# Performance work log

Hardware: AMD Instinct MI355X
Metric: run time of the kernel (lower is better)

## Reference

```python
import jax, jax.numpy as jnp
import numpy as np

B, C, F, H = 512, 80, 768, 256
EPS = 1e-5
THR = 0.5
SCALE = 1.0 / np.sqrt(H)


def _ln(z, g, b):
    m = jnp.mean(z, axis=-1, keepdims=True)
    v = jnp.mean((z - m) ** 2, axis=-1, keepdims=True)
    return (z - m) * jax.lax.rsqrt(v + EPS) * g + b


def setup_inputs() -> dict:
    key = jax.random.key(0)
    ks = jax.random.split(key, 12)
    w = 0.05  # weight scale for numerical sanity
    return {
        "x": jax.random.normal(ks[0], (B, C, H), jnp.float32),
        "visual_features": jax.random.normal(ks[1], (B, F), jnp.float32),
        "labels": jax.random.randint(ks[2], (B, C), 0, 2, jnp.int32),
        # visual_proj: Linear(F,H) + LayerNorm(H)
        "Wp": jax.random.normal(ks[3], (F, H), jnp.float32) * w,
        "bp": jnp.zeros((H,), jnp.float32),
        "gp": jnp.ones((H,), jnp.float32),
        "bep": jnp.zeros((H,), jnp.float32),
        # per-class extractors: stacked Linear(H,H) + LayerNorm(H)
        "Wc": jax.random.normal(ks[4], (C, H, H), jnp.float32) * w,
        "bc": jnp.zeros((C, H), jnp.float32),
        "gc": jnp.ones((C, H), jnp.float32),
        "bec": jnp.zeros((C, H), jnp.float32),
        # attention projections
        "Wq": jax.random.normal(ks[5], (H, H), jnp.float32) * w,
        "bq": jnp.zeros((H,), jnp.float32),
        "Wk": jax.random.normal(ks[6], (H, H), jnp.float32) * w,
        "bk": jnp.zeros((H,), jnp.float32),
        "Wv": jax.random.normal(ks[7], (H, H), jnp.float32) * w,
        "bv": jnp.zeros((H,), jnp.float32),
        "Wo": jax.random.normal(ks[8], (H, H), jnp.float32) * w,
        "bo": jnp.zeros((H,), jnp.float32),
    }


def reference(x, visual_features, labels, Wp, bp, gp, bep, Wc, bc, gc, bec,
              Wq, bq, Wk, bk, Wv, bv, Wo, bo):
    # visual_proj: Linear + LN + ReLU  -> (B,H)
    vis = jax.nn.relu(_ln(visual_features @ Wp + bp, gp, bep))
    # per-class extractor ensemble fused into one batched GEMM -> (B,C,H)
    z = jnp.einsum('bh,chk->bck', vis, Wc) + bc
    class_feats = jax.nn.relu(_ln(z, gc, bec))
    x = x + class_feats
    q = x @ Wq + bq
    k = x @ Wk + bk
    v = x @ Wv + bv
    scores = jnp.einsum('bch,bdh->bcd', q, k) * SCALE  # (B,C,C)
    scores = scores * (scores > THR).astype(scores.dtype)  # hard similarity mask
    label_mask = labels.astype(scores.dtype)[:, None, :] * 0.8 + 0.2
    scores = scores * label_mask
    attn = jax.nn.softmax(scores, axis=-1)
    out = jnp.einsum('bcd,bdh->bch', attn, v)
    return out @ Wo + bo
```

## Files before the change

### kernel.cpp

```cpp
#include <hip/hip_runtime.h>
#include <hip/hip_bf16.h>
#include <math.h>

#define Bq 512
#define Cq 80
#define Fq 768
#define Hq 256

constexpr float EPS   = 1e-5f;
constexpr float THR   = 0.5f;
constexpr float SCALE = 0.0625f;

using f32x4 = __attribute__((ext_vector_type(4))) float;
using s16x8 = __attribute__((ext_vector_type(8))) short;
using s16x4 = __attribute__((ext_vector_type(4))) short;

#define MFMA16 __builtin_amdgcn_mfma_f32_16x16x32_bf16


__device__ __forceinline__ float waveReduceSum(float v) {
#pragma unroll
  for (int m = 32; m >= 1; m >>= 1) v += __shfl_xor(v, m);
  return v;
}

__device__ __forceinline__ float bfu(unsigned short v) {
  return __uint_as_float(((unsigned)v) << 16);
}

__device__ __forceinline__ unsigned short f2bf(float f) {
  __hip_bfloat16 h = __float2bfloat16(f);
  return *reinterpret_cast<unsigned short*>(&h);
}

__device__ __forceinline__ int packOff(int tile, int kk8, int g, int l15, int e) {
  return ((tile * 8 + kk8) * 4 + g) * 128 + l15 * 8 + e;
}

__global__ __launch_bounds__(256) void k_setup(
    const float* __restrict__ vf, const float* __restrict__ Wp,
    const float* __restrict__ bp, const float* __restrict__ gp,
    const float* __restrict__ bep,
    unsigned short* __restrict__ visPh, unsigned short* __restrict__ visPl,
    const float* __restrict__ Wq, const float* __restrict__ Wk,
    const float* __restrict__ bq, const float* __restrict__ bk,
    unsigned short* __restrict__ MTph, unsigned short* __restrict__ MTpl,
    float* __restrict__ w1, float* __restrict__ w2, float* __restrict__ cqk,
    const float* __restrict__ Wc, const float* __restrict__ Wv,
    const float* __restrict__ Wo,
    unsigned short* __restrict__ WcTph, unsigned short* __restrict__ WcTpl,
    unsigned short* __restrict__ WvTp, unsigned short* __restrict__ WoTp) {
  __shared__ float smA[Fq];
  __shared__ float red[4], redB[4], redC[4];
  const int blk = blockIdx.x;

  if (blk < 512) {
    const int b = blk, h = threadIdx.x;
    for (int i = h; i < Fq; i += 256) smA[i] = vf[b * Fq + i];
    __syncthreads();
    float acc = bp[h];
    for (int f = 0; f < Fq; f++) acc = fmaf(smA[f], Wp[f * Hq + h], acc);
    const int w = h >> 6, lane = h & 63;
    float s = waveReduceSum(acc);
    if (lane == 0) red[w] = s;
    __syncthreads();
    const float mean = (red[0] + red[1] + red[2] + red[3]) * (1.0f / Hq);
    __syncthreads();
    const float d = acc - mean;
    s = waveReduceSum(d * d);
    if (lane == 0) red[w] = s;
    __syncthreads();
    const float var = (red[0] + red[1] + red[2] + red[3]) * (1.0f / Hq);
    float y = d * rsqrtf(var + EPS) * gp[h] + bep[h];
    y = fmaxf(y, 0.0f);
    const unsigned short hb = f2bf(y);
    const int off = packOff(b >> 4, h >> 5, (h & 31) >> 3, b & 15, h & 7);
    visPh[off] = hb;
    visPl[off] = f2bf(y - bfu(hb));
  } else if (blk < 768) {
    const int i = blk - 512, j = threadIdx.x;
    const int wv = j >> 6, lane = j & 63;
    smA[j] = Wq[i * Hq + j];
    __syncthreads();
    float acc = 0.f;
    const float* wkr = Wk + (size_t)j * Hq;
    for (int h = 0; h < Hq; h += 4) {
      const float4 a = *reinterpret_cast<const float4*>(&smA[h]);
      const float4 bb = *reinterpret_cast<const float4*>(&wkr[h]);
      acc = fmaf(a.x, bb.x, fmaf(a.y, bb.y, fmaf(a.z, bb.z, fmaf(a.w, bb.w, acc))));
    }
    const unsigned short hb = f2bf(acc);
    const int off = packOff(j >> 4, i >> 5, (i & 31) >> 3, j & 15, i & 7);
    MTph[off] = hb;
    MTpl[off] = f2bf(acc - bfu(hb));
    float p1 = smA[j] * bk[j];
    float p2 = Wk[(size_t)i * Hq + j] * bq[j];
    float p3 = bq[j] * bk[j];
    p1 = waveReduceSum(p1);
    p2 = waveReduceSum(p2);
    p3 = waveReduceSum(p3);
    if (lane == 0) { red[wv] = p1; redB[wv] = p2; redC[wv] = p3; }
    __syncthreads();
    if (j == 0) {
      w1[i] = red[0] + red[1] + red[2] + red[3];
      w2[i] = redB[0] + redB[1] + redB[2] + redB[3];
      if (i == 0) *cqk = redC[0] + redC[1] + redC[2] + redC[3];
    }
  } else {
    const int NWc = Cq * 32 * 256;
    const int NTOT = NWc + 2 * 32 * 256;
    for (int idx = (blk - 768) * 256 + threadIdx.x; idx < NTOT; idx += 1024 * 256) {
      if (idx < NWc) {
        const int c = idx >> 13, k8 = (idx >> 8) & 31, n = idx & 255;
        const float* src = Wc + (size_t)c * 65536 + (size_t)k8 * 8 * 256 + n;
        s16x8 hh, ll;
#pragma unroll
        for (int e = 0; e < 8; e++) {
          const float v = src[e * 256];
          const unsigned short hb = f2bf(v);
          hh[e] = (short)hb;
          ll[e] = (short)f2bf(v - bfu(hb));
        }
        const int off = c * 65536 + packOff(n >> 4, k8 >> 2, k8 & 3, n & 15, 0);
        *reinterpret_cast<s16x8*>(WcTph + off) = hh;
        *reinterpret_cast<s16x8*>(WcTpl + off) = ll;
      } else {
        const int r = idx - NWc;
        const int which = r >> 13;
        const int r2 = r & 8191;
        const int k8 = r2 >> 8, n = r2 & 255;
        const float* src = (which == 0 ? Wv : Wo) + (size_t)k8 * 8 * 256 + n;
        s16x8 hh;
#pragma unroll
        for (int e = 0; e < 8; e++) hh[e] = (short)f2bf(src[e * 256]);
        const int off = packOff(n >> 4, k8 >> 2, k8 & 3, n & 15, 0);
        *reinterpret_cast<s16x8*>((which == 0 ? WvTp : WoTp) + off) = hh;
      }
    }
  }
}

__global__ __launch_bounds__(256) void k_gemm1f(
    const unsigned short* __restrict__ visPh, const unsigned short* __restrict__ visPl,
    const unsigned short* __restrict__ WcTph, const unsigned short* __restrict__ WcTpl,
    const float* __restrict__ x, const float* __restrict__ bc,
    const float* __restrict__ gc, const float* __restrict__ bec,
    const float* __restrict__ w1, const float* __restrict__ w2,
    unsigned short* __restrict__ Xgh, unsigned short* __restrict__ Xgl,
    float* __restrict__ u, float* __restrict__ vv) {
  const int blk = blockIdx.x;
  const int mapped = (blk & 7) * 160 + (blk >> 3);
  const int c = mapped >> 4;
  const int bx = mapped & 15;
  const int b0 = bx * 32;
  const int tid = threadIdx.x;
  const int wvi = tid >> 6, lane = tid & 63;
  const int l15 = lane & 15, l4 = lane >> 4;

  __shared__ float Zs[32][268];

  f32x4 acc[2][4];
#pragma unroll
  for (int m = 0; m < 2; m++)
#pragma unroll
    for (int n = 0; n < 4; n++) acc[m][n] = (f32x4){0.f, 0.f, 0.f, 0.f};

  const unsigned short* Bh = WcTph + (size_t)c * 65536;
  const unsigned short* Bl = WcTpl + (size_t)c * 65536;

  for (int kk8 = 0; kk8 < 8; kk8++) {
    s16x8 ah[2], al[2], bh[4], bl[4];
#pragma unroll
    for (int m = 0; m < 2; m++) {
      const int off = packOff(bx * 2 + m, kk8, l4, l15, 0);
      ah[m] = *reinterpret_cast<const s16x8*>(visPh + off);
      al[m] = *reinterpret_cast<const s16x8*>(visPl + off);
    }
#pragma unroll
    for (int n = 0; n < 4; n++) {
      const int off = packOff(wvi * 4 + n, kk8, l4, l15, 0);
      bh[n] = *reinterpret_cast<const s16x8*>(Bh + off);
      bl[n] = *reinterpret_cast<const s16x8*>(Bl + off);
    }
#pragma unroll
    for (int m = 0; m < 2; m++)
#pragma unroll
      for (int n = 0; n < 4; n++) {
        acc[m][n] = MFMA16(ah[m], bh[n], acc[m][n], 0, 0, 0);
        acc[m][n] = MFMA16(ah[m], bl[n], acc[m][n], 0, 0, 0);
        acc[m][n] = MFMA16(al[m], bh[n], acc[m][n], 0, 0, 0);
      }
  }

#pragma unroll
  for (int m = 0; m < 2; m++)
#pragma unroll
    for (int n = 0; n < 4; n++) {
      const int col = wvi * 64 + n * 16 + l15;
      const float bcv = bc[c * Hq + col];
#pragma unroll
      for (int r = 0; r < 4; r++)
        Zs[m * 16 + l4 * 4 + r][col] = acc[m][n][r] + bcv;
    }
  __syncthreads();

  const int row = tid >> 3, sub = tid & 7;
  const int grow = b0 + row;
  const size_t xrow = ((size_t)grow * Cq + c) * Hq;
  float zz[32];
  float sum = 0.f, sumsq = 0.f;
#pragma unroll
  for (int kq = 0; kq < 8; kq++) {
    const float4 z = *reinterpret_cast<const float4*>(&Zs[row][sub * 4 + kq * 32]);
    zz[4 * kq + 0] = z.x; zz[4 * kq + 1] = z.y;
    zz[4 * kq + 2] = z.z; zz[4 * kq + 3] = z.w;
    sum += z.x + z.y + z.z + z.w;
    sumsq += z.x * z.x + z.y * z.y + z.z * z.z + z.w * z.w;
  }
#pragma unroll
  for (int msk = 4; msk >= 1; msk >>= 1) {
    sum += __shfl_xor(sum, msk);
    sumsq += __shfl_xor(sumsq, msk);
  }
  const float mean = sum * (1.0f / Hq);
  const float var = sumsq * (1.0f / Hq) - mean * mean;
  const float inv = rsqrtf(var + EPS);

  float pu = 0.f, pv = 0.f;
#pragma unroll
  for (int kq = 0; kq < 8; kq++) {
    const int col = sub * 4 + kq * 32;
    const float4 xv = *reinterpret_cast<const float4*>(&x[xrow + col]);
    const float xr[4] = {xv.x, xv.y, xv.z, xv.w};
    s16x4 hh, ll;
#pragma unroll
    for (int e = 0; e < 4; e++) {
      float tt = (zz[4 * kq + e] - mean) * inv * gc[c * Hq + col + e] + bec[c * Hq + col + e];
      tt = fmaxf(tt, 0.f);
      const float xp = xr[e] + tt;
      const unsigned short hb2 = f2bf(xp);
      hh[e] = (short)hb2;
      ll[e] = (short)f2bf(xp - bfu(hb2));
      pu = fmaf(xp, w1[col + e], pu);
      pv = fmaf(xp, w2[col + e], pv);
    }
    *reinterpret_cast<s16x4*>(Xgh + xrow + col) = hh;
    *reinterpret_cast<s16x4*>(Xgl + xrow + col) = ll;
  }
#pragma unroll
  for (int msk = 4; msk >= 1; msk >>= 1) {
    pu += __shfl_xor(pu, msk);
    pv += __shfl_xor(pv, msk);
  }
  if (sub == 0) {
    u[(size_t)grow * Cq + c] = pu;
    vv[(size_t)grow * Cq + c] = pv;
  }
}

__global__ __launch_bounds__(256) void k_gemm2p(
    unsigned short* Xh, unsigned short* Xl,
    const unsigned short* __restrict__ MTph, const unsigned short* __restrict__ MTpl,
    const unsigned short* __restrict__ WvTp, const float* __restrict__ bv,
    unsigned short* __restrict__ XMh, unsigned short* __restrict__ XMl,
    unsigned short* __restrict__ Vt) {
  __shared__ __attribute__((aligned(16))) unsigned short Xsh[32 * 264];
  __shared__ __attribute__((aligned(16))) unsigned short Xsl[32 * 264];
  __shared__ __attribute__((aligned(16))) unsigned short XMsh[8192];
  __shared__ __attribute__((aligned(16))) unsigned short XMsl[8192];
  __shared__ __attribute__((aligned(16))) unsigned short Vst[256 * 24];

  const int blk = blockIdx.x;
  const int r0 = blk * 32;
  const int tid = threadIdx.x;
  const int wvi = tid >> 6, lane = tid & 63;
  const int l15 = lane & 15, l4 = lane >> 4;

#pragma unroll
  for (int it = 0; it < 4; it++) {
    const int ch = it * 256 + tid;
    const int rr = ch >> 5, cc = ch & 31;
    const size_t gsrc = (size_t)(r0 + rr) * Hq + cc * 8;
    *reinterpret_cast<s16x8*>(&Xsh[rr * 264 + cc * 8]) =
        *reinterpret_cast<const s16x8*>(Xh + gsrc);
    *reinterpret_cast<s16x8*>(&Xsl[rr * 264 + cc * 8]) =
        *reinterpret_cast<const s16x8*>(Xl + gsrc);
  }
  __syncthreads();

  f32x4 acc[2][4];
#pragma unroll
  for (int m = 0; m < 2; m++)
#pragma unroll
    for (int n = 0; n < 4; n++) acc[m][n] = (f32x4){0.f, 0.f, 0.f, 0.f};

  for (int kk8 = 0; kk8 < 8; kk8++) {
    s16x8 ah[2], al[2], bh[4], bl[4];
#pragma unroll
    for (int m = 0; m < 2; m++) {
      const int lo = (m * 16 + l15) * 264 + kk8 * 32 + l4 * 8;
      ah[m] = *reinterpret_cast<const s16x8*>(&Xsh[lo]);
      al[m] = *reinterpret_cast<const s16x8*>(&Xsl[lo]);
    }
#pragma unroll
    for (int n = 0; n < 4; n++) {
      const int off = packOff(wvi * 4 + n, kk8, l4, l15, 0);
      bh[n] = *reinterpret_cast<const s16x8*>(MTph + off);
      bl[n] = *reinterpret_cast<const s16x8*>(MTpl + off);
    }
#pragma unroll
    for (int m = 0; m < 2; m++)
#pragma unroll
      for (int n = 0; n < 4; n++) {
        acc[m][n] = MFMA16(ah[m], bh[n], acc[m][n], 0, 0, 0);
        acc[m][n] = MFMA16(ah[m], bl[n], acc[m][n], 0, 0, 0);
        acc[m][n] = MFMA16(al[m], bh[n], acc[m][n], 0, 0, 0);
      }
  }

#pragma unroll
  for (int m = 0; m < 2; m++)
#pragma unroll
    for (int n = 0; n < 4; n++) {
      const int col = wvi * 64 + n * 16 + l15;
      const int kk8c = col >> 5, gc = (col & 31) >> 3, ec = col & 7;
#pragma unroll
      for (int r = 0; r < 4; r++) {
        const int off = ((m * 8 + kk8c) * 4 + gc) * 128 + (l4 * 4 + r) * 8 + ec;
        const float v = acc[m][n][r];
        const unsigned short hb = f2bf(v);
        XMsh[off] = hb;
        XMsl[off] = f2bf(v - bfu(hb));
      }
    }
  __syncthreads();

#pragma unroll
  for (int it = 0; it < 4; it++) {
    const int ch = it * 256 + tid;
    const size_t gdst = (size_t)blk * 8192 + ch * 8;
    *reinterpret_cast<s16x8*>(XMh + gdst) = *reinterpret_cast<const s16x8*>(&XMsh[ch * 8]);
    *reinterpret_cast<s16x8*>(XMl + gdst) = *reinterpret_cast<const s16x8*>(&XMsl[ch * 8]);
    const int l15c = ch & 15, g3 = (ch >> 4) & 3, kk = (ch >> 6) & 7, mm = ch >> 9;
    const int lsrc = (mm * 16 + l15c) * 264 + kk * 32 + g3 * 8;
    *reinterpret_cast<s16x8*>(Xh + gdst) = *reinterpret_cast<const s16x8*>(&Xsh[lsrc]);
    *reinterpret_cast<s16x8*>(Xl + gdst) = *reinterpret_cast<const s16x8*>(&Xsl[lsrc]);
  }

  for (int m = 0; m < 2; m++) {
    f32x4 vac[4];
#pragma unroll
    for (int n = 0; n < 4; n++) vac[n] = (f32x4){0.f, 0.f, 0.f, 0.f};
    for (int kk8 = 0; kk8 < 8; kk8++) {
      const int lo = (m * 16 + l15) * 264 + kk8 * 32 + l4 * 8;
      const s16x8 ah = *reinterpret_cast<const s16x8*>(&Xsh[lo]);
      const s16x8 al = *reinterpret_cast<const s16x8*>(&Xsl[lo]);
#pragma unroll
      for (int n = 0; n < 4; n++) {
        const s16x8 bh = *reinterpret_cast<const s16x8*>(
            WvTp + packOff(wvi * 4 + n, kk8, l4, l15, 0));
        vac[n] = MFMA16(ah, bh, vac[n], 0, 0, 0);
        vac[n] = MFMA16(al, bh, vac[n], 0, 0, 0);
      }
    }
#pragma unroll
    for (int n = 0; n < 4; n++) {
      const int col = (wvi * 4 + n) * 16 + l15;
      const float bvv = bv[col];
#pragma unroll
      for (int r = 0; r < 4; r++)
        Vst[col * 24 + l4 * 4 + r] = f2bf(vac[n][r] + bvv);
    }
    __syncthreads();
    {
      const int gt = blk * 2 + m;
      const int bb = gt / 5, ct = gt - bb * 5;
      const unsigned short* src = &Vst[tid * 24];
      const s16x8 va = *reinterpret_cast<const s16x8*>(src);
      const s16x8 vb2 = *reinterpret_cast<const s16x8*>(src + 8);
      const size_t ga = ((size_t)bb * Hq + tid) * Cq + ct * 16;
      *reinterpret_cast<s16x8*>(Vt + ga) = va;
      *reinterpret_cast<s16x8*>(Vt + ga + 8) = vb2;
    }
    __syncthreads();
  }
}

__global__ __launch_bounds__(320) void k_attn5(
    const unsigned short* __restrict__ XPh, const unsigned short* __restrict__ XPl,
    const unsigned short* __restrict__ XMh, const unsigned short* __restrict__ XMl,
    const unsigned short* __restrict__ Vt, const int* __restrict__ labels,
    const float* __restrict__ u, const float* __restrict__ vv,
    const float* __restrict__ cqk, const unsigned short* __restrict__ WoTp,
    const float* __restrict__ bo, float* __restrict__ out) {
  __shared__ unsigned short Pl_[80][104];
  __shared__ unsigned short Olds[80][264];
  __shared__ float us[80], vvs[80], lms[80];

  const int b = blockIdx.x, t = threadIdx.x;
  const int w = t >> 6, lane = t & 63;
  const int l15 = lane & 15, g = lane >> 4;

  if (t < 80) {
    us[t] = u[b * Cq + t];
    vvs[t] = vv[b * Cq + t];
    lms[t] = (float)labels[b * Cq + t] * 0.8f + 0.2f;
  }

  f32x4 sacc[5];
#pragma unroll
  for (int mt = 0; mt < 5; mt++) sacc[mt] = (f32x4){0.f, 0.f, 0.f, 0.f};

  for (int kk8 = 0; kk8 < 8; kk8++) {
    const int offB = packOff(b * 5 + w, kk8, g, l15, 0);
    const s16x8 bh = *reinterpret_cast<const s16x8*>(XMh + offB);
    const s16x8 bl = *reinterpret_cast<const s16x8*>(XMl + offB);
#pragma unroll
    for (int mt = 0; mt < 5; mt++) {
      const int offA = packOff(b * 5 + mt, kk8, g, l15, 0);
      const s16x8 ah = *reinterpret_cast<const s16x8*>(XPh + offA);
      const s16x8 al = *reinterpret_cast<const s16x8*>(XPl + offA);
      sacc[mt] = MFMA16(ah, bh, sacc[mt], 0, 0, 0);
      sacc[mt] = MFMA16(ah, bl, sacc[mt], 0, 0, 0);
      sacc[mt] = MFMA16(al, bh, sacc[mt], 0, 0, 0);
    }
  }
  __syncthreads();

  const int i = 16 * w + l15;
  const float ui = us[i];
  const float cq = *cqk;
  float p[5][4];
  float mx = -1e30f;
#pragma unroll
  for (int mt = 0; mt < 5; mt++)
#pragma unroll
    for (int r = 0; r < 4; r++) {
      const int j = 16 * mt + 4 * g + r;
      float sc = (sacc[mt][r] + ui + vvs[j] + cq) * SCALE;
      sc = (sc > THR) ? sc : 0.0f;
      sc *= lms[j];
      p[mt][r] = sc;
      mx = fmaxf(mx, sc);
    }
  mx = fmaxf(mx, __shfl_xor(mx, 16));
  mx = fmaxf(mx, __shfl_xor(mx, 32));
  float sum = 0.f;
#pragma unroll
  for (int mt = 0; mt < 5; mt++)
#pragma unroll
    for (int r = 0; r < 4; r++) {
      const float e = __expf(p[mt][r] - mx);
      p[mt][r] = e;
      sum += e;
    }
  sum += __shfl_xor(sum, 16);
  sum += __shfl_xor(sum, 32);
  const float inv = 1.0f / sum;

#pragma unroll
  for (int mt = 0; mt < 5; mt++) {
    uint2 pk;
    pk.x = (unsigned)f2bf(p[mt][0] * inv) | ((unsigned)f2bf(p[mt][1] * inv) << 16);
    pk.y = (unsigned)f2bf(p[mt][2] * inv) | ((unsigned)f2bf(p[mt][3] * inv) << 16);
    *reinterpret_cast<uint2*>(reinterpret_cast<char*>(&Pl_[i][0]) + 32 * mt + 8 * g) = pk;
  }
  if (t < 160) {
    const uint4 z = {0u, 0u, 0u, 0u};
    *reinterpret_cast<uint4*>(reinterpret_cast<char*>(&Pl_[t >> 1][0]) + 160 + 16 * (t & 1)) = z;
  }
  __syncthreads();

  s16x8 pa[3];
#pragma unroll
  for (int ks = 0; ks < 3; ks++)
    pa[ks] = *reinterpret_cast<const s16x8*>(
        reinterpret_cast<const char*>(&Pl_[i][0]) + 64 * ks + 16 * g);

  f32x4 oacc[16];
#pragma unroll
  for (int n = 0; n < 16; n++) oacc[n] = (f32x4){0.f, 0.f, 0.f, 0.f};

  const size_t vbase = (size_t)b * Hq * Cq;
#pragma unroll 4
  for (int n = 0; n < 16; n++) {
    const size_t hrow = vbase + (size_t)(16 * n + l15) * Cq + 8 * g;
#pragma unroll
    for (int ks = 0; ks < 3; ks++) {
      const s16x8 vb = *reinterpret_cast<const s16x8*>(Vt + hrow + 32 * ks);
      oacc[n] = MFMA16(pa[ks], vb, oacc[n], 0, 0, 0);
    }
  }

#pragma unroll
  for (int n = 0; n < 16; n++)
#pragma unroll
    for (int r = 0; r < 4; r++)
      Olds[16 * w + 4 * g + r][16 * n + l15] = f2bf(oacc[n][r]);

  f32x4 acc2[16];
#pragma unroll
  for (int n = 0; n < 16; n++) acc2[n] = (f32x4){0.f, 0.f, 0.f, 0.f};

  for (int ks = 0; ks < 8; ks++) {
    const s16x8 af = *reinterpret_cast<const s16x8*>(
        reinterpret_cast<const char*>(&Olds[16 * w + l15][0]) + 64 * ks + 16 * g);
#pragma unroll
    for (int n = 0; n < 16; n++) {
      const s16x8 bf = *reinterpret_cast<const s16x8*>(WoTp + packOff(n, ks, g, l15, 0));
      acc2[n] = MFMA16(af, bf, acc2[n], 0, 0, 0);
    }
  }

#pragma unroll
  for (int n = 0; n < 16; n++) {
    const float bov = bo[16 * n + l15];
#pragma unroll
    for (int r = 0; r < 4; r++)
      out[((size_t)b * Cq + 16 * w + 4 * g + r) * Hq + 16 * n + l15] =
          acc2[n][r] + bov;
  }
}

extern "C" void kernel_launch(void* const* d_in, const int* in_sizes, int n_in,
                              void* d_out, int out_size, void* d_ws, size_t ws_size,
                              hipStream_t stream) {
  const float* x   = (const float*)d_in[0];
  const float* vf  = (const float*)d_in[1];
  const int*   lab = (const int*)d_in[2];
  const float* Wp  = (const float*)d_in[3];
  const float* bp  = (const float*)d_in[4];
  const float* gp  = (const float*)d_in[5];
  const float* bep = (const float*)d_in[6];
  const float* Wc  = (const float*)d_in[7];
  const float* bc  = (const float*)d_in[8];
  const float* gc  = (const float*)d_in[9];
  const float* bec = (const float*)d_in[10];
  const float* Wq  = (const float*)d_in[11];
  const float* bq_ = (const float*)d_in[12];
  const float* Wk  = (const float*)d_in[13];
  const float* bk_ = (const float*)d_in[14];
  const float* Wv  = (const float*)d_in[15];
  const float* bv_ = (const float*)d_in[16];
  const float* Wo  = (const float*)d_in[17];
  const float* bo_ = (const float*)d_in[18];
  float* out = (float*)d_out;
  (void)ws_size; (void)in_sizes; (void)n_in; (void)out_size;

  char* W = (char*)d_ws;
  unsigned short* Xh    = (unsigned short*)(W + 0);
  unsigned short* Xl    = (unsigned short*)(W + 20971520);
  unsigned short* WcTph = (unsigned short*)(W + 41943040);
  unsigned short* WcTpl = (unsigned short*)(W + 52428800);
  unsigned short* XMh   = (unsigned short*)(W + 41943040);
  unsigned short* XMl   = (unsigned short*)(W + 62914560);
  unsigned short* Vt    = (unsigned short*)(W + 83886080);
  unsigned short* visPh = (unsigned short*)(W + 104857600);
  unsigned short* visPl = (unsigned short*)(W + 105119744);
  unsigned short* MTph  = (unsigned short*)(W + 105381888);
  unsigned short* MTpl  = (unsigned short*)(W + 105512960);
  unsigned short* WvTp  = (unsigned short*)(W + 105644032);
  unsigned short* WoTp  = (unsigned short*)(W + 105775104);
  float* w1  = (float*)(W + 105906176);
  float* w2  = (float*)(W + 105907200);
  float* cqk = (float*)(W + 105908224);
  float* u   = (float*)(W + 105908480);
  float* vvv = (float*)(W + 106072320);

  k_setup<<<1792, 256, 0, stream>>>(vf, Wp, bp, gp, bep, visPh, visPl,
                                    Wq, Wk, bq_, bk_, MTph, MTpl, w1, w2, cqk,
                                    Wc, Wv, Wo, WcTph, WcTpl, WvTp, WoTp);
  k_gemm1f<<<1280, 256, 0, stream>>>(visPh, visPl, WcTph, WcTpl, x, bc, gc, bec,
                                     w1, w2, Xh, Xl, u, vvv);
  k_gemm2p<<<1280, 256, 0, stream>>>(Xh, Xl, MTph, MTpl, WvTp, bv_,
                                     XMh, XMl, Vt);
  k_attn5<<<Bq, 320, 0, stream>>>(Xh, Xl, XMh, XMl, Vt, lab, u, vvv, cqk,
                                  WoTp, bo_, out);
}
```

Before: 193.6 us.

## Split attention kernel into one-wave blocks per 16-row tile with remapped grid

The attention kernel now launches 2560 single-wave blocks, one per (batch, 16-row class tile), in place of 512 five-wave blocks. Block indices are remapped so that consecutive blocks spread across the eight XCD groups. Shared memory per block shrinks and u is read straight from global memory. The aim is better occupancy, finer load balancing and cheaper block-wide barriers. In exchange, each block redundantly reloads per-batch vectors and V tiles, so L2 traffic goes up.

After: 209.1 us. +8.0%, slower.

```diff
diff --git a/kernel.cpp b/kernel.cpp
--- a/kernel.cpp
+++ b/kernel.cpp
@@ -386,25 +386,28 @@
   }
 }
 
-__global__ __launch_bounds__(320) void k_attn5(
+__global__ __launch_bounds__(64) void k_attn8(
     const unsigned short* __restrict__ XPh, const unsigned short* __restrict__ XPl,
     const unsigned short* __restrict__ XMh, const unsigned short* __restrict__ XMl,
     const unsigned short* __restrict__ Vt, const int* __restrict__ labels,
     const float* __restrict__ u, const float* __restrict__ vv,
     const float* __restrict__ cqk, const unsigned short* __restrict__ WoTp,
     const float* __restrict__ bo, float* __restrict__ out) {
-  __shared__ unsigned short Pl_[80][104];
-  __shared__ unsigned short Olds[80][264];
-  __shared__ float us[80], vvs[80], lms[80];
-
-  const int b = blockIdx.x, t = threadIdx.x;
-  const int w = t >> 6, lane = t & 63;
+  __shared__ unsigned short Pl_[16][104];
+  __shared__ unsigned short Olds[16][264];
+  __shared__ float vvs[80], lms[80];
+
+  const int blk = blockIdx.x;
+  const int mapped = (blk & 7) * 320 + (blk >> 3);
+  const int b = mapped / 5;
+  const int w = mapped - b * 5;
+
+  const int lane = threadIdx.x;
   const int l15 = lane & 15, g = lane >> 4;
 
-  if (t < 80) {
-    us[t] = u[b * Cq + t];
-    vvs[t] = vv[b * Cq + t];
-    lms[t] = (float)labels[b * Cq + t] * 0.8f + 0.2f;
+  for (int j = lane; j < 80; j += 64) {
+    vvs[j] = vv[b * Cq + j];
+    lms[j] = (float)labels[b * Cq + j] * 0.8f + 0.2f;
   }
 
   f32x4 sacc[5];
@@ -428,7 +431,7 @@
   __syncthreads();
 
   const int i = 16 * w + l15;
-  const float ui = us[i];
+  const float ui = u[b * Cq + i];
   const float cq = *cqk;
   float p[5][4];
   float mx = -1e30f;
@@ -463,11 +466,12 @@
     uint2 pk;
     pk.x = (unsigned)f2bf(p[mt][0] * inv) | ((unsigned)f2bf(p[mt][1] * inv) << 16);
     pk.y = (unsigned)f2bf(p[mt][2] * inv) | ((unsigned)f2bf(p[mt][3] * inv) << 16);
-    *reinterpret_cast<uint2*>(reinterpret_cast<char*>(&Pl_[i][0]) + 32 * mt + 8 * g) = pk;
-  }
-  if (t < 160) {
+    *reinterpret_cast<uint2*>(reinterpret_cast<char*>(&Pl_[l15][0]) + 32 * mt + 8 * g) = pk;
+  }
+  if (lane < 32) {
     const uint4 z = {0u, 0u, 0u, 0u};
-    *reinterpret_cast<uint4*>(reinterpret_cast<char*>(&Pl_[t >> 1][0]) + 160 + 16 * (t & 1)) = z;
+    *reinterpret_cast<uint4*>(
+        reinterpret_cast<char*>(&Pl_[lane >> 1][0]) + 160 + 16 * (lane & 1)) = z;
   }
   __syncthreads();
 
@@ -475,7 +479,7 @@
 #pragma unroll
   for (int ks = 0; ks < 3; ks++)
     pa[ks] = *reinterpret_cast<const s16x8*>(
-        reinterpret_cast<const char*>(&Pl_[i][0]) + 64 * ks + 16 * g);
+        reinterpret_cast<const char*>(&Pl_[l15][0]) + 64 * ks + 16 * g);
 
   f32x4 oacc[16];
 #pragma unroll
@@ -496,7 +500,8 @@
   for (int n = 0; n < 16; n++)
 #pragma unroll
     for (int r = 0; r < 4; r++)
-      Olds[16 * w + 4 * g + r][16 * n + l15] = f2bf(oacc[n][r]);
+      Olds[4 * g + r][16 * n + l15] = f2bf(oacc[n][r]);
+  __syncthreads();
 
   f32x4 acc2[16];
 #pragma unroll
@@ -504,7 +509,7 @@
 
   for (int ks = 0; ks < 8; ks++) {
     const s16x8 af = *reinterpret_cast<const s16x8*>(
-        reinterpret_cast<const char*>(&Olds[16 * w + l15][0]) + 64 * ks + 16 * g);
+        reinterpret_cast<const char*>(&Olds[l15][0]) + 64 * ks + 16 * g);
 #pragma unroll
     for (int n = 0; n < 16; n++) {
       const s16x8 bf = *reinterpret_cast<const s16x8*>(WoTp + packOff(n, ks, g, l15, 0));
@@ -574,6 +579,6 @@
                                      w1, w2, Xh, Xl, u, vvv);
   k_gemm2p<<<1280, 256, 0, stream>>>(Xh, Xl, MTph, MTpl, WvTp, bv_,
                                      XMh, XMl, Vt);
-  k_attn5<<<Bq, 320, 0, stream>>>(Xh, Xl, XMh, XMl, Vt, lab, u, vvv, cqk,
-                                  WoTp, bo_, out);
-}
+  k_attn8<<<2560, 64, 0, stream>>>(Xh, Xl, XMh, XMl, Vt, lab, u, vvv, cqk,
+                                   WoTp, bo_, out);
+}
```

## Stage QK operand tiles through double-buffered LDS in attention kernel

Applied to the files above, without the earlier changes.

The QK^T score loop now loads each k-slice of the packed X/XM hi-lo tiles once per block, cooperatively across all waves, into a double-buffered shared-memory area. Global loads for the next slice are issued before the MFMAs on the current one. Previously every wave re-read all five A tiles from global memory. The shared buffer is then reused as the Olds staging area to limit LDS footprint, at the cost of a block barrier per k-step.

New measurement: 189.4 us (median of 2 runs). 1.02x faster.

```diff
diff --git a/kernel.cpp b/kernel.cpp
--- a/kernel.cpp
+++ b/kernel.cpp
@@ -386,20 +386,21 @@
   }
 }
 
-__global__ __launch_bounds__(320) void k_attn5(
+__global__ __launch_bounds__(320) void k_attn9(
     const unsigned short* __restrict__ XPh, const unsigned short* __restrict__ XPl,
     const unsigned short* __restrict__ XMh, const unsigned short* __restrict__ XMl,
     const unsigned short* __restrict__ Vt, const int* __restrict__ labels,
     const float* __restrict__ u, const float* __restrict__ vv,
     const float* __restrict__ cqk, const unsigned short* __restrict__ WoTp,
     const float* __restrict__ bo, float* __restrict__ out) {
-  __shared__ unsigned short Pl_[80][104];
-  __shared__ unsigned short Olds[80][264];
+  __shared__ __attribute__((aligned(16))) unsigned short areaA[21120];
+  __shared__ __attribute__((aligned(16))) unsigned short Pl_[80][104];
   __shared__ float us[80], vvs[80], lms[80];
 
   const int b = blockIdx.x, t = threadIdx.x;
   const int w = t >> 6, lane = t & 63;
   const int l15 = lane & 15, g = lane >> 4;
+  const int tb = b * 5;
 
   if (t < 80) {
     us[t] = u[b * Cq + t];
@@ -407,25 +408,65 @@
     lms[t] = (float)labels[b * Cq + t] * 0.8f + 0.2f;
   }
 
+#define LOADSLICE(dst, KK)                                                      \
+  {                                                                             \
+    _Pragma("unroll")                                                           \
+    for (int q = 0; q < 4; q++) {                                               \
+      const int j = 4 * w + q;                                                  \
+      const unsigned short* base = (j < 5) ? XPh : (j < 10) ? XPl               \
+                                   : (j < 15) ? XMh : XMl;                      \
+      const int tile = tb + (j % 5);                                            \
+      dst[q] = *reinterpret_cast<const s16x8*>(                                 \
+          base + (size_t)(tile * 8 + (KK)) * 512 + lane * 8);                   \
+    }                                                                           \
+  }
+#define WRITESLICE(src, BUF)                                                    \
+  {                                                                             \
+    _Pragma("unroll")                                                           \
+    for (int q = 0; q < 4; q++)                                                 \
+      *reinterpret_cast<s16x8*>(                                                \
+          &areaA[(BUF) * 10240 + (4 * w + q) * 512 + lane * 8]) = src[q];       \
+  }
+
   f32x4 sacc[5];
 #pragma unroll
   for (int mt = 0; mt < 5; mt++) sacc[mt] = (f32x4){0.f, 0.f, 0.f, 0.f};
 
-  for (int kk8 = 0; kk8 < 8; kk8++) {
-    const int offB = packOff(b * 5 + w, kk8, g, l15, 0);
-    const s16x8 bh = *reinterpret_cast<const s16x8*>(XMh + offB);
-    const s16x8 bl = *reinterpret_cast<const s16x8*>(XMl + offB);
-#pragma unroll
-    for (int mt = 0; mt < 5; mt++) {
-      const int offA = packOff(b * 5 + mt, kk8, g, l15, 0);
-      const s16x8 ah = *reinterpret_cast<const s16x8*>(XPh + offA);
-      const s16x8 al = *reinterpret_cast<const s16x8*>(XPl + offA);
-      sacc[mt] = MFMA16(ah, bh, sacc[mt], 0, 0, 0);
-      sacc[mt] = MFMA16(ah, bl, sacc[mt], 0, 0, 0);
-      sacc[mt] = MFMA16(al, bh, sacc[mt], 0, 0, 0);
-    }
-  }
+  s16x8 sA[4], sB[4];
+  LOADSLICE(sA, 0);
+  LOADSLICE(sB, 1);
+  WRITESLICE(sA, 0);
   __syncthreads();
+
+#define QKSTEP(K, LD, WR)                                                       \
+  {                                                                             \
+    if ((K) < 6) LOADSLICE(LD, (K) + 2);                                        \
+    const unsigned short* B0 = &areaA[((K) & 1) * 10240];                       \
+    const s16x8 bh = *reinterpret_cast<const s16x8*>(B0 + (10 + w) * 512 + lane * 8);  \
+    const s16x8 bl = *reinterpret_cast<const s16x8*>(B0 + (15 + w) * 512 + lane * 8);  \
+    _Pragma("unroll")                                                           \
+    for (int mt = 0; mt < 5; mt++) {                                            \
+      const s16x8 ah = *reinterpret_cast<const s16x8*>(B0 + mt * 512 + lane * 8);      \
+      const s16x8 al = *reinterpret_cast<const s16x8*>(B0 + (5 + mt) * 512 + lane * 8);\
+      sacc[mt] = MFMA16(ah, bh, sacc[mt], 0, 0, 0);                             \
+      sacc[mt] = MFMA16(ah, bl, sacc[mt], 0, 0, 0);                             \
+      sacc[mt] = MFMA16(al, bh, sacc[mt], 0, 0, 0);                             \
+    }                                                                           \
+    if ((K) < 7) WRITESLICE(WR, ((K) + 1) & 1);                                 \
+    __syncthreads();                                                            \
+  }
+
+  QKSTEP(0, sA, sB)
+  QKSTEP(1, sB, sA)
+  QKSTEP(2, sA, sB)
+  QKSTEP(3, sB, sA)
+  QKSTEP(4, sA, sB)
+  QKSTEP(5, sB, sA)
+  QKSTEP(6, sA, sB)
+  QKSTEP(7, sB, sA)
+#undef QKSTEP
+#undef LOADSLICE
+#undef WRITESLICE
 
   const int i = 16 * w + l15;
   const float ui = us[i];
@@ -492,6 +533,7 @@
     }
   }
 
+  unsigned short (*Olds)[264] = reinterpret_cast<unsigned short (*)[264]>(areaA);
 #pragma unroll
   for (int n = 0; n < 16; n++)
 #pragma unroll
@@ -574,6 +616,6 @@
                                      w1, w2, Xh, Xl, u, vvv);
   k_gemm2p<<<1280, 256, 0, stream>>>(Xh, Xl, MTph, MTpl, WvTp, bv_,
                                      XMh, XMl, Vt);
-  k_attn5<<<Bq, 320, 0, stream>>>(Xh, Xl, XMh, XMl, Vt, lab, u, vvv, cqk,
+  k_attn9<<<Bq, 320, 0, stream>>>(Xh, Xl, XMh, XMl, Vt, lab, u, vvv, cqk,
                                   WoTp, bo_, out);
 }
```
